# Kernel optimization log

Hardware: AMD Instinct MI355X
Metric: run time of the kernel (lower is better)

Reference implementation:

```python
import jax, jax.numpy as jnp
import numpy as np

HEADS = 16
SEGS = 8


def _rotate_half(x):
    x1, x2 = jnp.split(x, 2, axis=-1)
    return jnp.concatenate([-x2, x1], axis=-1)


def _split_heads(t, h):
    b, n, dim = t.shape
    d = dim // h
    return t.reshape(b, n, h, d).transpose(0, 2, 1, 3).reshape(b * h, n, d)


def _merge_heads(t, b, h):
    c, n, d = t.shape
    return t.reshape(b, h, n, d).transpose(0, 2, 1, 3).reshape(b, n, h * d)


def setup_inputs() -> dict:
    key = jax.random.key(0)
    ks = jax.random.split(key, 5)
    b, n, dim = 2, 4096, 1024
    x = jax.random.normal(ks[0], (b, n, dim), dtype=jnp.float32)
    w = lambda k: jax.random.normal(k, (dim, dim), dtype=jnp.float32) * 0.02
    return {
        'x': x,
        'Wq': w(ks[1]),
        'Wkv': w(ks[2]),
        'Wo': w(ks[3]),
        'bo': jnp.zeros((dim,), jnp.float32),
        'Wo0': w(ks[4]),
        'bo0': jnp.zeros((dim,), jnp.float32),
    }


def reference(x, Wq, Wkv, Wo, bo, Wo0, bo0):
    b, n, dim = x.shape
    h = HEADS
    d = dim // h
    s = SEGS
    m = n // s  # segment_len
    mask_value = -jnp.finfo(x.dtype).max

    q = _split_heads(x @ Wq, h)    # (b*h, n, d)
    kv = _split_heads(x @ Wkv, h)  # (b*h, n, d)  (serves as both keys and values)

    # rotary embedding (layer_num == 0 branch)
    inv_freq = 1.0 / (10000.0 ** (jnp.arange(0, d, 2, dtype=jnp.float32) / d))
    freqs = jnp.arange(n, dtype=jnp.float32)[:, None] * inv_freq[None, :]  # (n, d/2)
    rot = jnp.concatenate([freqs, freqs], axis=-1)[None]  # (1, n, d)
    cos, sin = jnp.cos(rot), jnp.sin(rot)
    q = q * cos + _rotate_half(q) * sin
    kv = kv * cos + _rotate_half(kv) * sin

    q = q * (d ** -0.5)

    qs = q.reshape(-1, s, m, d)   # (c, s, m, d)
    kvs = kv.reshape(-1, s, m, d)

    # overlapping windows: segment t paired with segment t+1 as kv context
    kvs_ccs = jnp.concatenate([kvs[:, :-1], kvs[:, 1:]], axis=2)  # (c, s-1, 2m, d)
    qs_ccs = qs[:, 1:]                                            # (c, s-1, m, d)

    # NOTE: original computes lkv = LayerNorm(kvs_ccs) but never uses it (dead code) -> omitted.

    lsim = jnp.einsum('csmd,csnd->csmn', qs_ccs, kvs_ccs)  # (c, s-1, m, 2m)
    causal = jnp.triu(jnp.ones((m, m), dtype=bool), 1)
    # causal mask only applied to second half of keys (the own segment t+1)
    lsim = jnp.concatenate(
        [lsim[..., :m], jnp.where(causal, mask_value, lsim[..., m:])], axis=-1)

    attn0 = jnp.einsum('csmd,csnd->csmn', qs[:, :1], kvs[:, :1])  # (c, 1, m, m)
    attn0 = jnp.where(causal, mask_value, attn0)

    attn0 = jax.nn.softmax(attn0, axis=-1)
    attn1 = jax.nn.softmax(lsim, axis=-1)

    out0 = jnp.einsum('csij,csjd->csid', attn0, kvs[:, :1]).reshape(-1, m, d)
    out1 = jnp.einsum('csij,csjd->csid', attn1, kvs_ccs).reshape(-1, (s - 1) * m, d)

    out0 = _merge_heads(out0, b, h) @ Wo0 + bo0  # (b, m, dim)
    out1 = _merge_heads(out1, b, h) @ Wo + bo    # (b, (s-1)*m, dim)
    return jnp.concatenate([out0, out1], axis=1)  # (b, n, dim)
```

## Files before the change

kernel.cpp:

```cpp
#include <hip/hip_runtime.h>
#include <hip/hip_bf16.h>
#include <float.h>

using bf16 = __hip_bfloat16;
typedef __attribute__((ext_vector_type(8))) short bf16x8;
typedef __attribute__((ext_vector_type(4))) float f32x4;
typedef __attribute__((ext_vector_type(16))) float f32x16;

#define DIM   1024
#define NSEQ  4096
#define BATCH 2
#define NH    16
#define HD    64
#define NSEG  8
#define MSEG  512
#define ROWS  (BATCH*NSEQ)
#define NC    (BATCH*NH)
#define QSCALE (0.125f * 1.44269504f)

__device__ __forceinline__ float fast_exp2(float x) {
    float r;
    asm volatile("v_exp_f32 %0, %1" : "=v"(r) : "v"(x));
    return r;
}

__device__ __forceinline__ void gload16(const bf16* g, bf16* l) {
    __builtin_amdgcn_global_load_lds((const __attribute__((address_space(1))) unsigned int*)g,
                                     (__attribute__((address_space(3))) unsigned int*)l, 16, 0, 0);
}

__global__ void k_rope_tab(float* __restrict__ cosT, float* __restrict__ sinT) {
    int idx = blockIdx.x * 256 + threadIdx.x;
    int t = idx >> 5, i = idx & 31;
    float freq = 1.0f / powf(10000.0f, (float)(2 * i) * (1.0f / 64.0f));
    float a = (float)t * freq;
    cosT[idx] = cosf(a);
    sinT[idx] = sinf(a);
}

__global__ void k_convert_x(const float* __restrict__ X, bf16* __restrict__ Xb) {
    int i = (blockIdx.x * 256 + threadIdx.x) * 4;
    float4 v = *(const float4*)&X[i];
    union { bf16 h[4]; uint2 u; } p;
    p.h[0] = __float2bfloat16(v.x);
    p.h[1] = __float2bfloat16(v.y);
    p.h[2] = __float2bfloat16(v.z);
    p.h[3] = __float2bfloat16(v.w);
    *(uint2*)&Xb[i] = p.u;
}

__global__ void k_transpose(const float* __restrict__ W, bf16* __restrict__ Wt) {
    __shared__ float tile[32][33];
    int bx = blockIdx.x * 32;
    int by = blockIdx.y * 32;
    int tx = threadIdx.x;
    for (int i = threadIdx.y; i < 32; i += 8)
        tile[i][tx] = W[(size_t)(by + i) * DIM + bx + tx];
    __syncthreads();
    for (int i = threadIdx.y; i < 32; i += 8)
        Wt[(size_t)(bx + i) * DIM + by + tx] = __float2bfloat16(tile[tx][i]);
}

__launch_bounds__(256, 4)
__global__ void k_gemm_qkv(const bf16* __restrict__ A, const bf16* __restrict__ Bq,
                           const bf16* __restrict__ Bkv, const float* __restrict__ cosT,
                           const float* __restrict__ sinT, bf16* __restrict__ Qb,
                           bf16* __restrict__ KVb) {
    __shared__ alignas(16) bf16 As[2][128 * 32];
    __shared__ alignas(16) bf16 Bs[2][128 * 32];
    const int K = DIM;
    int tid = threadIdx.x;
    int lane = tid & 63, wave = tid >> 6;
    int wr = (wave >> 1) * 64, wc = (wave & 1) * 64;
    int id = blockIdx.x;
    int xcd = id & 7, rank = id >> 3;
    int by = xcd * 8 + (rank >> 4);
    int bxx = rank & 15;
    int m0 = by * 128;
    bool isQ = (bxx < 8);
    const bf16* Bt = isQ ? Bq : Bkv;
    int n0 = (bxx & 7) * 128;
    int row = lane & 15, kk = (lane >> 4) * 8;
    int ch0 = wave * 128 + lane, ch1 = ch0 + 64;
    int r0 = ch0 >> 2, c0e = (ch0 & 3) * 8;
    int r1 = ch1 >> 2, c1e = (ch1 & 3) * 8;
    f32x4 acc[4][4] = {};
    gload16(&A[(size_t)(m0 + r0) * K + c0e], &As[0][wave * 1024]);
    gload16(&A[(size_t)(m0 + r1) * K + c1e], &As[0][wave * 1024 + 512]);
    gload16(&Bt[(size_t)(n0 + r0) * K + c0e], &Bs[0][wave * 1024]);
    gload16(&Bt[(size_t)(n0 + r1) * K + c1e], &Bs[0][wave * 1024 + 512]);
    __syncthreads();
    int cur = 0;
    for (int k0 = 0; k0 < K; k0 += 32) {
        int nxt = cur ^ 1;
        if (k0 + 32 < K) {
            gload16(&A[(size_t)(m0 + r0) * K + k0 + 32 + c0e], &As[nxt][wave * 1024]);
            gload16(&A[(size_t)(m0 + r1) * K + k0 + 32 + c1e], &As[nxt][wave * 1024 + 512]);
            gload16(&Bt[(size_t)(n0 + r0) * K + k0 + 32 + c0e], &Bs[nxt][wave * 1024]);
            gload16(&Bt[(size_t)(n0 + r1) * K + k0 + 32 + c1e], &Bs[nxt][wave * 1024 + 512]);
        }
        bf16x8 af[4], bfr[4];
#pragma unroll
        for (int mt = 0; mt < 4; ++mt) af[mt] = *(const bf16x8*)&As[cur][(wr + mt * 16 + row) * 32 + kk];
#pragma unroll
        for (int nt = 0; nt < 4; ++nt) bfr[nt] = *(const bf16x8*)&Bs[cur][(wc + nt * 16 + row) * 32 + kk];
#pragma unroll
        for (int mt = 0; mt < 4; ++mt)
#pragma unroll
            for (int nt = 0; nt < 4; ++nt)
                acc[mt][nt] = __builtin_amdgcn_mfma_f32_16x16x32_bf16(af[mt], bfr[nt], acc[mt][nt], 0, 0, 0);
        __syncthreads();
        cur = nxt;
    }
    int orow = (lane >> 4) * 4, ocol = lane & 15;
    int head_g = (n0 + wc) >> 6;
    float sc = isQ ? QSCALE : 1.0f;
    bf16* Cb = isQ ? Qb : KVb;
#pragma unroll
    for (int mt = 0; mt < 4; ++mt) {
#pragma unroll
        for (int i = 0; i < 4; ++i) {
            int rowg = m0 + wr + mt * 16 + orow + i;
            int t = rowg & (NSEQ - 1), bidx = rowg >> 12;
            int cch = bidx * NH + head_g;
            size_t base = ((size_t)cch * NSEQ + t) * HD;
#pragma unroll
            for (int nt = 0; nt < 2; ++nt) {
                int e = nt * 16 + ocol;
                float x1 = acc[mt][nt][i], x2 = acc[mt][nt + 2][i];
                float cv = cosT[t * 32 + e], sv = sinT[t * 32 + e];
                Cb[base + e]      = __float2bfloat16((x1 * cv - x2 * sv) * sc);
                Cb[base + e + 32] = __float2bfloat16((x2 * cv + x1 * sv) * sc);
            }
        }
    }
}

__launch_bounds__(256, 2)
__global__ void k_gemm_out(const bf16* __restrict__ A, const bf16* __restrict__ Bt0,
                           const bf16* __restrict__ Bt1, const float* __restrict__ bias0,
                           const float* __restrict__ bias1, float* __restrict__ C) {
    __shared__ alignas(16) bf16 As[2][128 * 32];
    __shared__ alignas(16) bf16 Bs[2][128 * 32];
    const int K = DIM;
    int tid = threadIdx.x;
    int lane = tid & 63, wave = tid >> 6;
    int wr = (wave >> 1) * 64, wc = (wave & 1) * 64;
    int id = blockIdx.x;
    int xcd = id & 7, rank = id >> 3;
    int by = xcd * 8 + (rank >> 3);
    int bx = rank & 7;
    int m0 = by * 128, n0 = bx * 128;
    bool first = (m0 & (NSEQ - 1)) < MSEG;
    const bf16* Bt = first ? Bt0 : Bt1;
    const float* bias = first ? bias0 : bias1;
    int row = lane & 15, kk = (lane >> 4) * 8;
    int ch0 = wave * 128 + lane, ch1 = ch0 + 64;
    int r0 = ch0 >> 2, c0e = (ch0 & 3) * 8;
    int r1 = ch1 >> 2, c1e = (ch1 & 3) * 8;
    f32x4 acc[4][4] = {};
    gload16(&A[(size_t)(m0 + r0) * K + c0e], &As[0][wave * 1024]);
    gload16(&A[(size_t)(m0 + r1) * K + c1e], &As[0][wave * 1024 + 512]);
    gload16(&Bt[(size_t)(n0 + r0) * K + c0e], &Bs[0][wave * 1024]);
    gload16(&Bt[(size_t)(n0 + r1) * K + c1e], &Bs[0][wave * 1024 + 512]);
    __syncthreads();
    int cur = 0;
    for (int k0 = 0; k0 < K; k0 += 32) {
        int nxt = cur ^ 1;
        if (k0 + 32 < K) {
            gload16(&A[(size_t)(m0 + r0) * K + k0 + 32 + c0e], &As[nxt][wave * 1024]);
            gload16(&A[(size_t)(m0 + r1) * K + k0 + 32 + c1e], &As[nxt][wave * 1024 + 512]);
            gload16(&Bt[(size_t)(n0 + r0) * K + k0 + 32 + c0e], &Bs[nxt][wave * 1024]);
            gload16(&Bt[(size_t)(n0 + r1) * K + k0 + 32 + c1e], &Bs[nxt][wave * 1024 + 512]);
        }
        bf16x8 af[4], bfr[4];
#pragma unroll
        for (int mt = 0; mt < 4; ++mt) af[mt] = *(const bf16x8*)&As[cur][(wr + mt * 16 + row) * 32 + kk];
#pragma unroll
        for (int nt = 0; nt < 4; ++nt) bfr[nt] = *(const bf16x8*)&Bs[cur][(wc + nt * 16 + row) * 32 + kk];
#pragma unroll
        for (int mt = 0; mt < 4; ++mt)
#pragma unroll
            for (int nt = 0; nt < 4; ++nt)
                acc[mt][nt] = __builtin_amdgcn_mfma_f32_16x16x32_bf16(af[mt], bfr[nt], acc[mt][nt], 0, 0, 0);
        __syncthreads();
        cur = nxt;
    }
    int orow = (lane >> 4) * 4, ocol = lane & 15;
#pragma unroll
    for (int mt = 0; mt < 4; ++mt)
#pragma unroll
        for (int nt = 0; nt < 4; ++nt) {
            float bv = bias[n0 + wc + nt * 16 + ocol];
#pragma unroll
            for (int i = 0; i < 4; ++i)
                C[(size_t)(m0 + wr + mt * 16 + orow + i) * DIM + n0 + wc + nt * 16 + ocol] = acc[mt][nt][i] + bv;
        }
}

__global__ void k_pack(const bf16* __restrict__ KVb, bf16* __restrict__ KVf) {
    __shared__ bf16 T[256][72];
    int c = blockIdx.y, t0 = blockIdx.x * 256;
    int tid = threadIdx.x;
    int r = tid >> 3, cc = (tid & 7) * 8;
#pragma unroll
    for (int it = 0; it < 8; ++it) {
        int row = it * 32 + r;
        *(bf16x8*)&T[row][cc] = *(const bf16x8*)&KVb[((size_t)c * NSEQ + t0 + row) * HD + cc];
    }
    __syncthreads();
    int lane = tid & 63, wave = tid >> 6;
    int hi = lane >> 5, lq = lane & 31;
    size_t base = (((size_t)c * 128 + (t0 >> 5)) * 8) * 512;
    for (int tl = wave * 2; tl < wave * 2 + 2; ++tl) {
        size_t tb = base + (size_t)tl * 4096;
#pragma unroll
        for (int f = 0; f < 4; ++f) {
            bf16x8 v = *(const bf16x8*)&T[tl * 32 + lq][f * 16 + hi * 8];
            *(bf16x8*)&KVf[tb + (size_t)f * 512 + lane * 8] = v;
        }
#pragma unroll
        for (int m = 0; m < 4; ++m) {
            int d0 = (m >> 1) * 32, sub = m & 1;
            union { bf16 h[8]; bf16x8 v; } pk;
#pragma unroll
            for (int j = 0; j < 8; ++j)
                pk.h[j] = T[tl * 32 + sub * 16 + hi * 8 + j][d0 + lq];
            *(bf16x8*)&KVf[tb + (size_t)(4 + m) * 512 + lane * 8] = pk.v;
        }
    }
}

__launch_bounds__(256, 4)
__global__ void k_attn(const bf16* __restrict__ Qb, const bf16* __restrict__ KVf,
                       bf16* __restrict__ Ob) {
    int lane = threadIdx.x & 63, wave = threadIdx.x >> 6;
    int hi = lane >> 5, lq = lane & 31;
    int id = blockIdx.x;
    int xcd = id & 7, rank = id >> 3;
    int c = xcd * 4 + (rank & 3);
    int hr = rank >> 2;
    int bx, seg;
    if (hr < 28) { bx = 3 - hr / 7; seg = 1 + hr % 7; }
    else         { seg = 0; bx = 31 - hr; }
    int i0 = bx * 128 + wave * 32;
    int bidx = c >> 4, head = c & 15;
    int tq = seg * MSEG + i0 + lq;
    const bf16* qptr = &Qb[((size_t)c * NSEQ + tq) * HD + hi * 8];
    bf16x8 qf[4];
#pragma unroll
    for (int dc = 0; dc < 4; ++dc) qf[dc] = *(const bf16x8*)&qptr[dc * 16];
    f32x16 o0 = {}, o1 = {};
    float mrun = -FLT_MAX, lrun = 0.f;
    int kvbase = (seg == 0) ? 0 : (seg - 1) * MSEG;
    int cstart = (seg == 0) ? 0 : MSEG;
    int cend = cstart + i0 + 32;
    int nT = cend >> 5;

    const bf16* fb = &KVf[((size_t)c * 128 + (kvbase >> 5)) * 4096 + lane * 8];

    bf16x8 ka0, ka1, ka2, ka3;
    f32x16 s;
    {
        bf16x8 k0 = *(const bf16x8*)&fb[0];
        bf16x8 k1 = *(const bf16x8*)&fb[512];
        bf16x8 k2 = *(const bf16x8*)&fb[1024];
        bf16x8 k3 = *(const bf16x8*)&fb[1536];
        if (nT > 1) {
            const bf16* p1 = fb + 4096;
            ka0 = *(const bf16x8*)&p1[0];
            ka1 = *(const bf16x8*)&p1[512];
            ka2 = *(const bf16x8*)&p1[1024];
            ka3 = *(const bf16x8*)&p1[1536];
        }
        f32x16 z = {};
        __builtin_amdgcn_s_setprio(1);
        z = __builtin_amdgcn_mfma_f32_32x32x16_bf16(k0, qf[0], z, 0, 0, 0);
        z = __builtin_amdgcn_mfma_f32_32x32x16_bf16(k1, qf[1], z, 0, 0, 0);
        z = __builtin_amdgcn_mfma_f32_32x32x16_bf16(k2, qf[2], z, 0, 0, 0);
        z = __builtin_amdgcn_mfma_f32_32x32x16_bf16(k3, qf[3], z, 0, 0, 0);
        __builtin_amdgcn_s_setprio(0);
        s = z;
    }

    for (int it = 0; it < nT; ++it) {
        int c0 = it * 32;
        const bf16* pv = fb + (size_t)it * 4096 + 2048;
        bf16x8 vf0 = *(const bf16x8*)&pv[0];
        bf16x8 vf1 = *(const bf16x8*)&pv[512];
        bf16x8 vf2 = *(const bf16x8*)&pv[1024];
        bf16x8 vf3 = *(const bf16x8*)&pv[1536];
        if (c0 + 31 >= cstart && c0 + 31 - cstart > i0) {
#pragma unroll
            for (int r = 0; r < 16; ++r) {
                int kvg = c0 + ((r & 3) + 8 * (r >> 2) + 4 * hi);
                if (kvg >= cstart && kvg - cstart > i0 + lq) s[r] = -FLT_MAX;
            }
        }
        float m8[8], m4[4];
#pragma unroll
        for (int r = 0; r < 8; ++r) m8[r] = fmaxf(s[2 * r], s[2 * r + 1]);
#pragma unroll
        for (int r = 0; r < 4; ++r) m4[r] = fmaxf(m8[2 * r], m8[2 * r + 1]);
        float vmax = fmaxf(fmaxf(m4[0], m4[1]), fmaxf(m4[2], m4[3]));
        vmax = fmaxf(vmax, __shfl_xor(vmax, 32));
        if (__any(vmax > mrun + 11.5f)) {
            float nm = fmaxf(mrun, vmax);
            float al = fast_exp2(mrun - nm);
#pragma unroll
            for (int r = 0; r < 16; ++r) { o0[r] *= al; o1[r] *= al; }
            lrun *= al;
            mrun = nm;
        }
        float p[16];
#pragma unroll
        for (int r = 0; r < 16; ++r) p[r] = fast_exp2(s[r] - mrun);
        if (it + 1 < nT) {
            f32x16 z = {};
            __builtin_amdgcn_s_setprio(1);
            z = __builtin_amdgcn_mfma_f32_32x32x16_bf16(ka0, qf[0], z, 0, 0, 0);
            z = __builtin_amdgcn_mfma_f32_32x32x16_bf16(ka1, qf[1], z, 0, 0, 0);
            z = __builtin_amdgcn_mfma_f32_32x32x16_bf16(ka2, qf[2], z, 0, 0, 0);
            z = __builtin_amdgcn_mfma_f32_32x32x16_bf16(ka3, qf[3], z, 0, 0, 0);
            __builtin_amdgcn_s_setprio(0);
            s = z;
            if (it + 2 < nT) {
                const bf16* pn = fb + (size_t)(it + 2) * 4096;
                ka0 = *(const bf16x8*)&pn[0];
                ka1 = *(const bf16x8*)&pn[512];
                ka2 = *(const bf16x8*)&pn[1024];
                ka3 = *(const bf16x8*)&pn[1536];
            }
        }
        float a8[8], a4[4];
#pragma unroll
        for (int r = 0; r < 8; ++r) a8[r] = p[2 * r] + p[2 * r + 1];
#pragma unroll
        for (int r = 0; r < 4; ++r) a4[r] = a8[2 * r] + a8[2 * r + 1];
        lrun += (a4[0] + a4[1]) + (a4[2] + a4[3]);
        unsigned pk[8];
#pragma unroll
        for (int k = 0; k < 8; ++k) {
            union { bf16 h[2]; unsigned u; } cv;
            cv.h[0] = __float2bfloat16(p[2 * k]);
            cv.h[1] = __float2bfloat16(p[2 * k + 1]);
            pk[k] = cv.u;
        }
        unsigned u0 = hi ? pk[0] : pk[2];
        unsigned u1 = hi ? pk[1] : pk[3];
        unsigned u2 = hi ? pk[4] : pk[6];
        unsigned u3 = hi ? pk[5] : pk[7];
        unsigned w0 = (unsigned)__shfl_xor((int)u0, 32);
        unsigned w1 = (unsigned)__shfl_xor((int)u1, 32);
        unsigned w2 = (unsigned)__shfl_xor((int)u2, 32);
        unsigned w3 = (unsigned)__shfl_xor((int)u3, 32);
        union { unsigned u[4]; bf16x8 v; } b0, b1;
        b0.u[0] = hi ? w0 : pk[0];
        b0.u[1] = hi ? w1 : pk[1];
        b0.u[2] = hi ? pk[2] : w0;
        b0.u[3] = hi ? pk[3] : w1;
        b1.u[0] = hi ? w2 : pk[4];
        b1.u[1] = hi ? w3 : pk[5];
        b1.u[2] = hi ? pk[6] : w2;
        b1.u[3] = hi ? pk[7] : w3;
        __builtin_amdgcn_s_setprio(1);
        o0 = __builtin_amdgcn_mfma_f32_32x32x16_bf16(vf0, b0.v, o0, 0, 0, 0);
        o1 = __builtin_amdgcn_mfma_f32_32x32x16_bf16(vf2, b0.v, o1, 0, 0, 0);
        o0 = __builtin_amdgcn_mfma_f32_32x32x16_bf16(vf1, b1.v, o0, 0, 0, 0);
        o1 = __builtin_amdgcn_mfma_f32_32x32x16_bf16(vf3, b1.v, o1, 0, 0, 0);
        __builtin_amdgcn_s_setprio(0);
    }
    lrun += __shfl_xor(lrun, 32);
    float inv = 1.0f / lrun;
    size_t obase = ((size_t)bidx * NSEQ + tq) * DIM + head * HD;
#pragma unroll
    for (int dt = 0; dt < 2; ++dt)
#pragma unroll
        for (int a = 0; a < 4; ++a) {
            union { bf16 h[4]; uint2 u; } pkd;
            const f32x16& ov = dt ? o1 : o0;
#pragma unroll
            for (int i = 0; i < 4; ++i) pkd.h[i] = __float2bfloat16(ov[4 * a + i] * inv);
            *(uint2*)&Ob[obase + dt * 32 + 8 * a + 4 * hi] = pkd.u;
        }
}

extern "C" void kernel_launch(void* const* d_in, const int* in_sizes, int n_in,
                              void* d_out, int out_size, void* d_ws, size_t ws_size,
                              hipStream_t stream) {
    const float* x   = (const float*)d_in[0];
    const float* Wq  = (const float*)d_in[1];
    const float* Wkv = (const float*)d_in[2];
    const float* Wo  = (const float*)d_in[3];
    const float* bo  = (const float*)d_in[4];
    const float* Wo0 = (const float*)d_in[5];
    const float* bo0 = (const float*)d_in[6];
    float* out = (float*)d_out;

    char* ws = (char*)d_ws;
    size_t off = 0;
    auto alloc = [&](size_t bytes) { void* p = ws + off; off += (bytes + 255) & ~(size_t)255; return p; };
    float* cosT = (float*)alloc((size_t)NSEQ * 32 * 4);
    float* sinT = (float*)alloc((size_t)NSEQ * 32 * 4);
    bf16* Xb    = (bf16*)alloc((size_t)ROWS * DIM * 2);
    bf16* WqT   = (bf16*)alloc((size_t)DIM * DIM * 2);
    bf16* WkvT  = (bf16*)alloc((size_t)DIM * DIM * 2);
    bf16* WoT   = (bf16*)alloc((size_t)DIM * DIM * 2);
    bf16* Wo0T  = (bf16*)alloc((size_t)DIM * DIM * 2);
    bf16* Qb    = (bf16*)alloc((size_t)NC * NSEQ * HD * 2);
    bf16* KVb   = (bf16*)alloc((size_t)NC * NSEQ * HD * 2);
    bf16* KVf   = (bf16*)alloc((size_t)NC * 128 * 4096 * 2);
    bf16* Ob    = (bf16*)alloc((size_t)ROWS * DIM * 2);

    hipLaunchKernelGGL(k_rope_tab, dim3(NSEQ * 32 / 256), dim3(256), 0, stream, cosT, sinT);
    hipLaunchKernelGGL(k_convert_x, dim3(ROWS * DIM / 4 / 256), dim3(256), 0, stream, x, Xb);
    hipLaunchKernelGGL(k_transpose, dim3(32, 32), dim3(32, 8), 0, stream, Wq, WqT);
    hipLaunchKernelGGL(k_transpose, dim3(32, 32), dim3(32, 8), 0, stream, Wkv, WkvT);
    hipLaunchKernelGGL(k_transpose, dim3(32, 32), dim3(32, 8), 0, stream, Wo, WoT);
    hipLaunchKernelGGL(k_transpose, dim3(32, 32), dim3(32, 8), 0, stream, Wo0, Wo0T);

    hipLaunchKernelGGL(k_gemm_qkv, dim3(1024), dim3(256), 0, stream, Xb, WqT, WkvT, cosT, sinT, Qb, KVb);
    hipLaunchKernelGGL(k_pack, dim3(16, 32), dim3(256), 0, stream, KVb, KVf);

    hipLaunchKernelGGL(k_attn, dim3(1024), dim3(256), 0, stream, Qb, KVf, Ob);

    hipLaunchKernelGGL(k_gemm_out, dim3(512), dim3(256), 0, stream, Ob, Wo0T, WoT, bo0, bo, out);
}
```

Measured before the change: 161.4 us.

## Fuse KV packing into QKV GEMM epilogue and retile output GEMM

The QKV GEMM epilogue now stages each wave's rotary-applied tile in shared memory. Q is written with coalesced 16-byte stores, and the KV tile is written directly in the packed fragment layout the attention kernel reads. This removes the separate k_pack kernel and the KVb round trip through global memory. The output GEMM moves to 128x64 tiles with 1024 blocks and higher occupancy bounds, trading more A-tile reloads for better CU utilisation.

```diff
diff --git a/kernel.cpp b/kernel.cpp
--- a/kernel.cpp
+++ b/kernel.cpp
@@ -65,12 +65,14 @@
 __global__ void k_gemm_qkv(const bf16* __restrict__ A, const bf16* __restrict__ Bq,
                            const bf16* __restrict__ Bkv, const float* __restrict__ cosT,
                            const float* __restrict__ sinT, bf16* __restrict__ Qb,
-                           bf16* __restrict__ KVb) {
-    __shared__ alignas(16) bf16 As[2][128 * 32];
-    __shared__ alignas(16) bf16 Bs[2][128 * 32];
+                           bf16* __restrict__ KVf) {
+    __shared__ alignas(16) bf16 SH[18432];
+    bf16* AsB = SH;
+    bf16* BsB = SH + 8192;
     const int K = DIM;
     int tid = threadIdx.x;
     int lane = tid & 63, wave = tid >> 6;
+    int hi = lane >> 5, lq = lane & 31;
     int wr = (wave >> 1) * 64, wc = (wave & 1) * 64;
     int id = blockIdx.x;
     int xcd = id & 7, rank = id >> 3;
@@ -85,10 +87,114 @@
     int r0 = ch0 >> 2, c0e = (ch0 & 3) * 8;
     int r1 = ch1 >> 2, c1e = (ch1 & 3) * 8;
     f32x4 acc[4][4] = {};
+    gload16(&A[(size_t)(m0 + r0) * K + c0e], &AsB[wave * 1024]);
+    gload16(&A[(size_t)(m0 + r1) * K + c1e], &AsB[wave * 1024 + 512]);
+    gload16(&Bt[(size_t)(n0 + r0) * K + c0e], &BsB[wave * 1024]);
+    gload16(&Bt[(size_t)(n0 + r1) * K + c1e], &BsB[wave * 1024 + 512]);
+    __syncthreads();
+    int cur = 0;
+    for (int k0 = 0; k0 < K; k0 += 32) {
+        int nxt = cur ^ 1;
+        if (k0 + 32 < K) {
+            gload16(&A[(size_t)(m0 + r0) * K + k0 + 32 + c0e], &AsB[nxt * 4096 + wave * 1024]);
+            gload16(&A[(size_t)(m0 + r1) * K + k0 + 32 + c1e], &AsB[nxt * 4096 + wave * 1024 + 512]);
+            gload16(&Bt[(size_t)(n0 + r0) * K + k0 + 32 + c0e], &BsB[nxt * 4096 + wave * 1024]);
+            gload16(&Bt[(size_t)(n0 + r1) * K + k0 + 32 + c1e], &BsB[nxt * 4096 + wave * 1024 + 512]);
+        }
+        bf16x8 af[4], bfr[4];
+#pragma unroll
+        for (int mt = 0; mt < 4; ++mt) af[mt] = *(const bf16x8*)&AsB[cur * 4096 + (wr + mt * 16 + row) * 32 + kk];
+#pragma unroll
+        for (int nt = 0; nt < 4; ++nt) bfr[nt] = *(const bf16x8*)&BsB[cur * 4096 + (wc + nt * 16 + row) * 32 + kk];
+#pragma unroll
+        for (int mt = 0; mt < 4; ++mt)
+#pragma unroll
+            for (int nt = 0; nt < 4; ++nt)
+                acc[mt][nt] = __builtin_amdgcn_mfma_f32_16x16x32_bf16(af[mt], bfr[nt], acc[mt][nt], 0, 0, 0);
+        __syncthreads();
+        cur = nxt;
+    }
+    bf16* Tw = SH + wave * (64 * 72);
+    int orow = (lane >> 4) * 4, ocol = lane & 15;
+    int head_g = (n0 + wc) >> 6;
+    float sc = isQ ? QSCALE : 1.0f;
+    int bidx = (m0 + wr) >> 12;
+    int tbase = (m0 + wr) & (NSEQ - 1);
+    int cch = bidx * NH + head_g;
+#pragma unroll
+    for (int mt = 0; mt < 4; ++mt) {
+#pragma unroll
+        for (int i = 0; i < 4; ++i) {
+            int rl = mt * 16 + orow + i;
+            int t = tbase + rl;
+#pragma unroll
+            for (int nt = 0; nt < 2; ++nt) {
+                int e = nt * 16 + ocol;
+                float x1 = acc[mt][nt][i], x2 = acc[mt][nt + 2][i];
+                float cv = cosT[t * 32 + e], sv = sinT[t * 32 + e];
+                Tw[rl * 72 + e]      = __float2bfloat16((x1 * cv - x2 * sv) * sc);
+                Tw[rl * 72 + e + 32] = __float2bfloat16((x2 * cv + x1 * sv) * sc);
+            }
+        }
+    }
+    if (isQ) {
+        int rsub = lane >> 3, dg = (lane & 7) * 8;
+        size_t qbase = ((size_t)cch * NSEQ + tbase) * HD;
+#pragma unroll
+        for (int rr = 0; rr < 8; ++rr) {
+            int rl = rr * 8 + rsub;
+            *(uint4*)&Qb[qbase + (size_t)rl * HD + dg] = *(const uint4*)&Tw[rl * 72 + dg];
+        }
+    } else {
+        size_t kvfbase = ((size_t)cch * 128 + (tbase >> 5)) * 4096;
+#pragma unroll
+        for (int st = 0; st < 2; ++st) {
+            size_t tb = kvfbase + (size_t)st * 4096;
+#pragma unroll
+            for (int f = 0; f < 4; ++f)
+                *(uint4*)&KVf[tb + f * 512 + lane * 8] =
+                    *(const uint4*)&Tw[(st * 32 + lq) * 72 + f * 16 + hi * 8];
+#pragma unroll
+            for (int m = 0; m < 4; ++m) {
+                int d0 = (m >> 1) * 32, sb = m & 1;
+                union { bf16 h[8]; uint4 u; } pk;
+#pragma unroll
+                for (int j = 0; j < 8; ++j)
+                    pk.h[j] = Tw[(st * 32 + sb * 16 + hi * 8 + j) * 72 + d0 + lq];
+                *(uint4*)&KVf[tb + (size_t)(4 + m) * 512 + lane * 8] = pk.u;
+            }
+        }
+    }
+}
+
+__launch_bounds__(256, 4)
+__global__ void k_gemm_out(const bf16* __restrict__ A, const bf16* __restrict__ Bt0,
+                           const bf16* __restrict__ Bt1, const float* __restrict__ bias0,
+                           const float* __restrict__ bias1, float* __restrict__ C) {
+    __shared__ alignas(16) bf16 As[2][128 * 32];
+    __shared__ alignas(16) bf16 Bs[2][64 * 32];
+    const int K = DIM;
+    int tid = threadIdx.x;
+    int lane = tid & 63, wave = tid >> 6;
+    int wr = (wave >> 1) * 64, wc = (wave & 1) * 32;
+    int id = blockIdx.x;
+    int xcd = id & 7, rank = id >> 3;
+    int by = xcd * 8 + (rank >> 4);
+    int bx = rank & 15;
+    int m0 = by * 128, n0 = bx * 64;
+    bool first = (m0 & (NSEQ - 1)) < MSEG;
+    const bf16* Bt = first ? Bt0 : Bt1;
+    const float* bias = first ? bias0 : bias1;
+    int row = lane & 15, kk = (lane >> 4) * 8;
+    int ch0 = wave * 128 + lane, ch1 = ch0 + 64;
+    int r0 = ch0 >> 2, c0e = (ch0 & 3) * 8;
+    int r1 = ch1 >> 2, c1e = (ch1 & 3) * 8;
+    int cb = wave * 64 + lane;
+    int rb = cb >> 2, cbe = (cb & 3) * 8;
+    f32x4 acc[4][2] = {};
     gload16(&A[(size_t)(m0 + r0) * K + c0e], &As[0][wave * 1024]);
     gload16(&A[(size_t)(m0 + r1) * K + c1e], &As[0][wave * 1024 + 512]);
-    gload16(&Bt[(size_t)(n0 + r0) * K + c0e], &Bs[0][wave * 1024]);
-    gload16(&Bt[(size_t)(n0 + r1) * K + c1e], &Bs[0][wave * 1024 + 512]);
+    gload16(&Bt[(size_t)(n0 + rb) * K + cbe], &Bs[0][wave * 512]);
     __syncthreads();
     int cur = 0;
     for (int k0 = 0; k0 < K; k0 += 32) {
@@ -96,139 +202,31 @@
         if (k0 + 32 < K) {
             gload16(&A[(size_t)(m0 + r0) * K + k0 + 32 + c0e], &As[nxt][wave * 1024]);
             gload16(&A[(size_t)(m0 + r1) * K + k0 + 32 + c1e], &As[nxt][wave * 1024 + 512]);
-            gload16(&Bt[(size_t)(n0 + r0) * K + k0 + 32 + c0e], &Bs[nxt][wave * 1024]);
-            gload16(&Bt[(size_t)(n0 + r1) * K + k0 + 32 + c1e], &Bs[nxt][wave * 1024 + 512]);
-        }
-        bf16x8 af[4], bfr[4];
+            gload16(&Bt[(size_t)(n0 + rb) * K + k0 + 32 + cbe], &Bs[nxt][wave * 512]);
+        }
+        bf16x8 af[4], bfr[2];
 #pragma unroll
         for (int mt = 0; mt < 4; ++mt) af[mt] = *(const bf16x8*)&As[cur][(wr + mt * 16 + row) * 32 + kk];
 #pragma unroll
-        for (int nt = 0; nt < 4; ++nt) bfr[nt] = *(const bf16x8*)&Bs[cur][(wc + nt * 16 + row) * 32 + kk];
+        for (int nt = 0; nt < 2; ++nt) bfr[nt] = *(const bf16x8*)&Bs[cur][(wc + nt * 16 + row) * 32 + kk];
 #pragma unroll
         for (int mt = 0; mt < 4; ++mt)
 #pragma unroll
-            for (int nt = 0; nt < 4; ++nt)
+            for (int nt = 0; nt < 2; ++nt)
                 acc[mt][nt] = __builtin_amdgcn_mfma_f32_16x16x32_bf16(af[mt], bfr[nt], acc[mt][nt], 0, 0, 0);
         __syncthreads();
         cur = nxt;
     }
     int orow = (lane >> 4) * 4, ocol = lane & 15;
-    int head_g = (n0 + wc) >> 6;
-    float sc = isQ ? QSCALE : 1.0f;
-    bf16* Cb = isQ ? Qb : KVb;
-#pragma unroll
-    for (int mt = 0; mt < 4; ++mt) {
-#pragma unroll
-        for (int i = 0; i < 4; ++i) {
-            int rowg = m0 + wr + mt * 16 + orow + i;
-            int t = rowg & (NSEQ - 1), bidx = rowg >> 12;
-            int cch = bidx * NH + head_g;
-            size_t base = ((size_t)cch * NSEQ + t) * HD;
-#pragma unroll
-            for (int nt = 0; nt < 2; ++nt) {
-                int e = nt * 16 + ocol;
-                float x1 = acc[mt][nt][i], x2 = acc[mt][nt + 2][i];
-                float cv = cosT[t * 32 + e], sv = sinT[t * 32 + e];
-                Cb[base + e]      = __float2bfloat16((x1 * cv - x2 * sv) * sc);
-                Cb[base + e + 32] = __float2bfloat16((x2 * cv + x1 * sv) * sc);
-            }
-        }
-    }
-}
-
-__launch_bounds__(256, 2)
-__global__ void k_gemm_out(const bf16* __restrict__ A, const bf16* __restrict__ Bt0,
-                           const bf16* __restrict__ Bt1, const float* __restrict__ bias0,
-                           const float* __restrict__ bias1, float* __restrict__ C) {
-    __shared__ alignas(16) bf16 As[2][128 * 32];
-    __shared__ alignas(16) bf16 Bs[2][128 * 32];
-    const int K = DIM;
-    int tid = threadIdx.x;
-    int lane = tid & 63, wave = tid >> 6;
-    int wr = (wave >> 1) * 64, wc = (wave & 1) * 64;
-    int id = blockIdx.x;
-    int xcd = id & 7, rank = id >> 3;
-    int by = xcd * 8 + (rank >> 3);
-    int bx = rank & 7;
-    int m0 = by * 128, n0 = bx * 128;
-    bool first = (m0 & (NSEQ - 1)) < MSEG;
-    const bf16* Bt = first ? Bt0 : Bt1;
-    const float* bias = first ? bias0 : bias1;
-    int row = lane & 15, kk = (lane >> 4) * 8;
-    int ch0 = wave * 128 + lane, ch1 = ch0 + 64;
-    int r0 = ch0 >> 2, c0e = (ch0 & 3) * 8;
-    int r1 = ch1 >> 2, c1e = (ch1 & 3) * 8;
-    f32x4 acc[4][4] = {};
-    gload16(&A[(size_t)(m0 + r0) * K + c0e], &As[0][wave * 1024]);
-    gload16(&A[(size_t)(m0 + r1) * K + c1e], &As[0][wave * 1024 + 512]);
-    gload16(&Bt[(size_t)(n0 + r0) * K + c0e], &Bs[0][wave * 1024]);
-    gload16(&Bt[(size_t)(n0 + r1) * K + c1e], &Bs[0][wave * 1024 + 512]);
-    __syncthreads();
-    int cur = 0;
-    for (int k0 = 0; k0 < K; k0 += 32) {
-        int nxt = cur ^ 1;
-        if (k0 + 32 < K) {
-            gload16(&A[(size_t)(m0 + r0) * K + k0 + 32 + c0e], &As[nxt][wave * 1024]);
-            gload16(&A[(size_t)(m0 + r1) * K + k0 + 32 + c1e], &As[nxt][wave * 1024 + 512]);
-            gload16(&Bt[(size_t)(n0 + r0) * K + k0 + 32 + c0e], &Bs[nxt][wave * 1024]);
-            gload16(&Bt[(size_t)(n0 + r1) * K + k0 + 32 + c1e], &Bs[nxt][wave * 1024 + 512]);
-        }
-        bf16x8 af[4], bfr[4];
-#pragma unroll
-        for (int mt = 0; mt < 4; ++mt) af[mt] = *(const bf16x8*)&As[cur][(wr + mt * 16 + row) * 32 + kk];
-#pragma unroll
-        for (int nt = 0; nt < 4; ++nt) bfr[nt] = *(const bf16x8*)&Bs[cur][(wc + nt * 16 + row) * 32 + kk];
-#pragma unroll
-        for (int mt = 0; mt < 4; ++mt)
-#pragma unroll
-            for (int nt = 0; nt < 4; ++nt)
-                acc[mt][nt] = __builtin_amdgcn_mfma_f32_16x16x32_bf16(af[mt], bfr[nt], acc[mt][nt], 0, 0, 0);
-        __syncthreads();
-        cur = nxt;
-    }
-    int orow = (lane >> 4) * 4, ocol = lane & 15;
 #pragma unroll
     for (int mt = 0; mt < 4; ++mt)
 #pragma unroll
-        for (int nt = 0; nt < 4; ++nt) {
+        for (int nt = 0; nt < 2; ++nt) {
             float bv = bias[n0 + wc + nt * 16 + ocol];
 #pragma unroll
             for (int i = 0; i < 4; ++i)
                 C[(size_t)(m0 + wr + mt * 16 + orow + i) * DIM + n0 + wc + nt * 16 + ocol] = acc[mt][nt][i] + bv;
         }
-}
-
-__global__ void k_pack(const bf16* __restrict__ KVb, bf16* __restrict__ KVf) {
-    __shared__ bf16 T[256][72];
-    int c = blockIdx.y, t0 = blockIdx.x * 256;
-    int tid = threadIdx.x;
-    int r = tid >> 3, cc = (tid & 7) * 8;
-#pragma unroll
-    for (int it = 0; it < 8; ++it) {
-        int row = it * 32 + r;
-        *(bf16x8*)&T[row][cc] = *(const bf16x8*)&KVb[((size_t)c * NSEQ + t0 + row) * HD + cc];
-    }
-    __syncthreads();
-    int lane = tid & 63, wave = tid >> 6;
-    int hi = lane >> 5, lq = lane & 31;
-    size_t base = (((size_t)c * 128 + (t0 >> 5)) * 8) * 512;
-    for (int tl = wave * 2; tl < wave * 2 + 2; ++tl) {
-        size_t tb = base + (size_t)tl * 4096;
-#pragma unroll
-        for (int f = 0; f < 4; ++f) {
-            bf16x8 v = *(const bf16x8*)&T[tl * 32 + lq][f * 16 + hi * 8];
-            *(bf16x8*)&KVf[tb + (size_t)f * 512 + lane * 8] = v;
-        }
-#pragma unroll
-        for (int m = 0; m < 4; ++m) {
-            int d0 = (m >> 1) * 32, sub = m & 1;
-            union { bf16 h[8]; bf16x8 v; } pk;
-#pragma unroll
-            for (int j = 0; j < 8; ++j)
-                pk.h[j] = T[tl * 32 + sub * 16 + hi * 8 + j][d0 + lq];
-            *(bf16x8*)&KVf[tb + (size_t)(4 + m) * 512 + lane * 8] = pk.v;
-        }
-    }
 }
 
 __launch_bounds__(256, 4)
@@ -408,7 +406,6 @@
     bf16* WoT   = (bf16*)alloc((size_t)DIM * DIM * 2);
     bf16* Wo0T  = (bf16*)alloc((size_t)DIM * DIM * 2);
     bf16* Qb    = (bf16*)alloc((size_t)NC * NSEQ * HD * 2);
-    bf16* KVb   = (bf16*)alloc((size_t)NC * NSEQ * HD * 2);
     bf16* KVf   = (bf16*)alloc((size_t)NC * 128 * 4096 * 2);
     bf16* Ob    = (bf16*)alloc((size_t)ROWS * DIM * 2);
 
@@ -419,10 +416,9 @@
     hipLaunchKernelGGL(k_transpose, dim3(32, 32), dim3(32, 8), 0, stream, Wo, WoT);
     hipLaunchKernelGGL(k_transpose, dim3(32, 32), dim3(32, 8), 0, stream, Wo0, Wo0T);
 
-    hipLaunchKernelGGL(k_gemm_qkv, dim3(1024), dim3(256), 0, stream, Xb, WqT, WkvT, cosT, sinT, Qb, KVb);
-    hipLaunchKernelGGL(k_pack, dim3(16, 32), dim3(256), 0, stream, KVb, KVf);
+    hipLaunchKernelGGL(k_gemm_qkv, dim3(1024), dim3(256), 0, stream, Xb, WqT, WkvT, cosT, sinT, Qb, KVf);
 
     hipLaunchKernelGGL(k_attn, dim3(1024), dim3(256), 0, stream, Qb, KVf, Ob);
 
-    hipLaunchKernelGGL(k_gemm_out, dim3(512), dim3(256), 0, stream, Ob, Wo0T, WoT, bo0, bo, out);
-}
+    hipLaunchKernelGGL(k_gemm_out, dim3(1024), dim3(256), 0, stream, Ob, Wo0T, WoT, bo0, bo, out);
+}
```

Measured after the change: 158.2 us. About the same (-1.9%).
